# Kernel tuning notes

Measured on AMD Instinct MI355X. Metric: run time of the kernel, lower is better.

The kernel has to match this reference:

```python
import jax, jax.numpy as jnp
import numpy as np

D, N, M = 256, 8192, 8192
DISTANCE_THRESH = 0.8


def setup_inputs() -> dict:
    key = jax.random.key(0)
    k0, k1 = jax.random.split(key)
    d0 = jax.random.normal(k0, (D, N), dtype=jnp.float32)
    d1 = jax.random.normal(k1, (D, M), dtype=jnp.float32)
    # descriptors are L2-normalized along the feature dim (cosine similarity,
    # consistent with the 2*(1-sim) squared-distance formula in the module)
    d0 = d0 / jnp.linalg.norm(d0, axis=0, keepdims=True)
    d1 = d1 / jnp.linalg.norm(d1, axis=0, keepdims=True)
    return {"descriptors0": d0, "descriptors1": d1}


def reference(descriptors0, descriptors1):
    # nn_sim: [N, M] similarity matrix
    nn_sim = jnp.einsum('dn,dm->nm', descriptors0, descriptors1)
    nn_dist_01 = jnp.max(nn_sim, axis=1)          # [N]
    nn_idx_01 = jnp.argmax(nn_sim, axis=1)        # [N]
    nn_idx_10 = jnp.argmax(nn_sim, axis=0)        # [M]
    nn_dist = 2.0 * (1.0 - nn_dist_01)            # squared L2 dist for unit vecs
    ids1 = jnp.arange(nn_sim.shape[0])
    mask = ids1 == nn_idx_10[nn_idx_01]           # mutual NN check
    if DISTANCE_THRESH > 0.0:
        mask = mask & (nn_dist <= DISTANCE_THRESH ** 2)
    matches = jnp.where(mask, nn_idx_01, -1)
    scores = jnp.where(mask, (nn_dist + 1.0) / 2.0, 0.0)
    return matches, scores
```

## Files before the change

kernel.cpp:

```cpp
#include <hip/hip_runtime.h>
#include <hip/hip_bf16.h>

typedef __attribute__((ext_vector_type(8))) short short8;
typedef __attribute__((ext_vector_type(4))) float floatx4;
typedef unsigned int u32;

#define D_DIM 256
#define TCOLS 64
#define TILES 8
#define IDX_BITS 0x1FFFu
#define VAL_MASK 0xFFFFE000u


__device__ inline unsigned short f2bf_rne(float f) {
  u32 u = __float_as_uint(f);
  u32 r = (u + 0x7FFFu + ((u >> 16) & 1u)) >> 16;
  return (unsigned short)r;
}

__device__ inline u32 umax(u32 a, u32 b) { return a > b ? a : b; }

__device__ inline void async_ld16(const void* g, void* l) {
  __builtin_amdgcn_global_load_lds((const __attribute__((address_space(1))) void*)g,
                                   (__attribute__((address_space(3))) void*)l, 16, 0, 0);
}


__global__ __launch_bounds__(256) void transpose_cast(const float* __restrict__ d0,
                                                      const float* __restrict__ d1,
                                                      unsigned short* __restrict__ At,
                                                      unsigned short* __restrict__ Bt,
                                                      int C, u32* __restrict__ best, int init_n) {
  const float* src = blockIdx.z ? d1 : d0;
  unsigned short* dst = blockIdx.z ? Bt : At;
  const int tid = threadIdx.x;
  const int d = blockIdx.x * 64 + (tid & 63);
  const int chunk = blockIdx.y * 4 + (tid >> 6);
  const int f0 = chunk * 8;
  float v[8];
#pragma unroll
  for (int u = 0; u < 8; ++u) v[u] = src[(size_t)(f0 + u) * C + d];
  short8 o;
#pragma unroll
  for (int u = 0; u < 8; ++u) o[u] = (short)f2bf_rne(v[u]);
  *(short8*)(dst + (size_t)d * D_DIM + f0) = o;
  if (blockIdx.z == 0 && blockIdx.y == 0) {
    int i = blockIdx.x * 256 + tid;
    if (i < init_n) best[i] = 0u;
  }
}

__global__ __launch_bounds__(256, 1) void gemm_reduce(const unsigned short* __restrict__ At,
                                                      const unsigned short* __restrict__ Bt,
                                                      u32* __restrict__ best01,
                                                      u32* __restrict__ best10) {
  __shared__ alignas(16) unsigned short sB[2][TCOLS * D_DIM];
  __shared__ u32 ldsCol[2][TCOLS];

  const int tid  = threadIdx.x;
  const int wave = tid >> 6;
  const int lane = tid & 63;
  const int quad = lane >> 4;
  const int l15  = lane & 15;
  const int n0   = blockIdx.x * 256;
  const int mg0  = blockIdx.y * (TILES * TCOLS);
  const int rbase = n0 + wave * 64;

  if (tid < 2 * TCOLS) ldsCol[tid >> 6][tid & 63] = 0u;

  {
    const unsigned short* src = Bt + (size_t)mg0 * D_DIM;
#pragma unroll
    for (int c = 0; c < 8; ++c) {
      int slot = c * 256 + tid;
      int r = slot >> 5, cc = slot & 31;
      int ccg = (cc & 24) | ((cc ^ r) & 7);
      async_ld16(src + (size_t)r * D_DIM + ccg * 8, (unsigned short*)sB[0] + slot * 8);
    }
  }

  short8 af[4][8];
#pragma unroll
  for (int t = 0; t < 4; ++t)
#pragma unroll
    for (int kc = 0; kc < 8; ++kc)
      af[t][kc] = *(const short8*)(At + (size_t)(rbase + t * 16 + l15) * D_DIM + kc * 32 + quad * 8);

  u32 rbk[16];
#pragma unroll
  for (int s = 0; s < 16; ++s) rbk[s] = 0u;

  __syncthreads();

  for (int mt = 0; mt < TILES; ++mt) {
    const int m0 = mg0 + mt * TCOLS;
    if (mt + 1 < TILES) {
      const unsigned short* src = Bt + (size_t)(m0 + TCOLS) * D_DIM;
      unsigned short* dstb = (unsigned short*)sB[(mt + 1) & 1];
#pragma unroll
      for (int c = 0; c < 8; ++c) {
        int slot = c * 256 + tid;
        int r = slot >> 5, cc = slot & 31;
        int ccg = (cc & 24) | ((cc ^ r) & 7);
        async_ld16(src + (size_t)r * D_DIM + ccg * 8, dstb + slot * 8);
      }
    }

    floatx4 acc[4][4];
#pragma unroll
    for (int i = 0; i < 4; ++i)
#pragma unroll
      for (int j = 0; j < 4; ++j)
        acc[i][j] = (floatx4){2.0f, 2.0f, 2.0f, 2.0f};

    const unsigned short* sb = (const unsigned short*)sB[mt & 1];
#pragma unroll
    for (int kc = 0; kc < 8; ++kc) {
      short8 bfr[4];
#pragma unroll
      for (int j = 0; j < 4; ++j) {
        int c2 = j * 16 + l15;
        int ch = kc * 4 + quad;
        int chg = (ch & 24) | ((ch ^ c2) & 7);
        bfr[j] = *(const short8*)(sb + c2 * D_DIM + chg * 8);
      }
#pragma unroll
      for (int i = 0; i < 4; ++i)
#pragma unroll
        for (int j = 0; j < 4; ++j)
          acc[i][j] = __builtin_amdgcn_mfma_f32_16x16x32_bf16(af[i][kc], bfr[j], acc[i][j], 0, 0, 0);
    }

    u32 cb[4] = {0u, 0u, 0u, 0u};
    u32 colpay[4];
#pragma unroll
    for (int j = 0; j < 4; ++j) colpay[j] = (~(u32)(m0 + j * 16 + l15)) & IDX_BITS;
#pragma unroll
    for (int i = 0; i < 4; ++i)
#pragma unroll
      for (int r = 0; r < 4; ++r) {
        u32 rowpay = (~(u32)(rbase + i * 16 + quad * 4 + r)) & IDX_BITS;
        u32 rb = rbk[i * 4 + r];
#pragma unroll
        for (int j = 0; j < 4; ++j) {
          u32 u = __float_as_uint(acc[i][j][r]) & VAL_MASK;
          rb = umax(rb, u | colpay[j]);
          cb[j] = umax(cb[j], u | rowpay);
        }
        rbk[i * 4 + r] = rb;
      }
#pragma unroll
    for (int j = 0; j < 4; ++j) {
      u32 b = cb[j];
      b = umax(b, (u32)__shfl_xor((int)b, 16, 64));
      b = umax(b, (u32)__shfl_xor((int)b, 32, 64));
      if (quad == 0) atomicMax(&ldsCol[mt & 1][j * 16 + l15], b);
    }
    __syncthreads();
    if (tid < TCOLS) {
      u32 g = ldsCol[mt & 1][tid];
      ldsCol[mt & 1][tid] = 0u;
      atomicMax(&best10[m0 + tid], g);
    }
  }

#pragma unroll
  for (int i = 0; i < 4; ++i)
#pragma unroll
    for (int r = 0; r < 4; ++r) {
      u32 b = rbk[i * 4 + r];
      b = umax(b, (u32)__shfl_xor((int)b, 1, 64));
      b = umax(b, (u32)__shfl_xor((int)b, 2, 64));
      b = umax(b, (u32)__shfl_xor((int)b, 4, 64));
      b = umax(b, (u32)__shfl_xor((int)b, 8, 64));
      if (l15 == 0) atomicMax(&best01[rbase + i * 16 + quad * 4 + r], b);
    }
}

__global__ void finalize(const u32* __restrict__ best01, const u32* __restrict__ best10,
                         float* __restrict__ out, int N) {
  int n = blockIdx.x * blockDim.x + threadIdx.x;
  if (n >= N) return;
  u32 k = best01[n];
  int idx01 = (int)((~k) & IDX_BITS);
  float sim = __uint_as_float(k & VAL_MASK) - 2.0f;
  int idx10 = (int)((~best10[idx01]) & IDX_BITS);
  float dist = 2.0f - 2.0f * sim;
  bool ok = (idx10 == n) && (dist <= 0.64f);
  out[n]     = ok ? (float)idx01 : -1.0f;
  out[N + n] = ok ? 1.5f - sim : 0.0f;
}


extern "C" void kernel_launch(void* const* d_in, const int* in_sizes, int n_in,
                              void* d_out, int out_size, void* d_ws, size_t ws_size,
                              hipStream_t stream) {
  (void)n_in; (void)out_size; (void)ws_size;
  const float* d0 = (const float*)d_in[0];
  const float* d1 = (const float*)d_in[1];
  const int N = in_sizes[0] / D_DIM;
  const int M = in_sizes[1] / D_DIM;

  u32* best01 = (u32*)d_ws;
  u32* best10 = best01 + N;
  unsigned short* At = (unsigned short*)(best10 + M);
  unsigned short* Bt = At + (size_t)N * D_DIM;
  float* out = (float*)d_out;

  hipLaunchKernelGGL(transpose_cast, dim3(N / 64, 8, 2), dim3(256), 0, stream,
                     d0, d1, At, Bt, N, best01, N + M);
  hipLaunchKernelGGL(gemm_reduce, dim3(N / 256, M / (TILES * TCOLS)), dim3(256), 0, stream,
                     At, Bt, best01, best10);
  hipLaunchKernelGGL(finalize, dim3(N / 256), dim3(256), 0, stream, best01, best10, out, N);
}
```

Baseline: 122.8 us.

## Fuse descriptor0 bf16 conversion into GEMM and drop LDS column reduction

The GEMM kernel now reads descriptors0 as fp32 straight from global memory and converts it to bf16 in registers. This removes the separate transpose/cast pass and the workspace buffer for that operand; only descriptors1 is still pre-transposed. The per-block LDS stage for column maxima is also removed, so each wave issues its column-max atomics directly to global memory. The trade-offs are twice as many bytes read for A, from strided fp32 loads repeated by every column-block. Global atomic traffic on best10 is also about four times higher.

```diff
diff --git a/kernel.cpp b/kernel.cpp
--- a/kernel.cpp
+++ b/kernel.cpp
@@ -26,13 +26,9 @@
 }
 
 
-__global__ __launch_bounds__(256) void transpose_cast(const float* __restrict__ d0,
-                                                      const float* __restrict__ d1,
-                                                      unsigned short* __restrict__ At,
-                                                      unsigned short* __restrict__ Bt,
-                                                      int C, u32* __restrict__ best, int init_n) {
-  const float* src = blockIdx.z ? d1 : d0;
-  unsigned short* dst = blockIdx.z ? Bt : At;
+__global__ __launch_bounds__(256) void transpose_cast(const float* __restrict__ src,
+                                                      unsigned short* __restrict__ dst, int C,
+                                                      u32* __restrict__ best, int init_n) {
   const int tid = threadIdx.x;
   const int d = blockIdx.x * 64 + (tid & 63);
   const int chunk = blockIdx.y * 4 + (tid >> 6);
@@ -44,18 +40,18 @@
 #pragma unroll
   for (int u = 0; u < 8; ++u) o[u] = (short)f2bf_rne(v[u]);
   *(short8*)(dst + (size_t)d * D_DIM + f0) = o;
-  if (blockIdx.z == 0 && blockIdx.y == 0) {
+  if (blockIdx.y == 0) {
     int i = blockIdx.x * 256 + tid;
     if (i < init_n) best[i] = 0u;
   }
 }
 
-__global__ __launch_bounds__(256, 1) void gemm_reduce(const unsigned short* __restrict__ At,
+__global__ __launch_bounds__(256, 1) void gemm_reduce(const float* __restrict__ A,
                                                       const unsigned short* __restrict__ Bt,
                                                       u32* __restrict__ best01,
-                                                      u32* __restrict__ best10) {
+                                                      u32* __restrict__ best10,
+                                                      int N) {
   __shared__ alignas(16) unsigned short sB[2][TCOLS * D_DIM];
-  __shared__ u32 ldsCol[2][TCOLS];
 
   const int tid  = threadIdx.x;
   const int wave = tid >> 6;
@@ -66,8 +62,6 @@
   const int mg0  = blockIdx.y * (TILES * TCOLS);
   const int rbase = n0 + wave * 64;
 
-  if (tid < 2 * TCOLS) ldsCol[tid >> 6][tid & 63] = 0u;
-
   {
     const unsigned short* src = Bt + (size_t)mg0 * D_DIM;
 #pragma unroll
@@ -83,8 +77,15 @@
 #pragma unroll
   for (int t = 0; t < 4; ++t)
 #pragma unroll
-    for (int kc = 0; kc < 8; ++kc)
-      af[t][kc] = *(const short8*)(At + (size_t)(rbase + t * 16 + l15) * D_DIM + kc * 32 + quad * 8);
+    for (int kc = 0; kc < 8; ++kc) {
+      const int row = rbase + t * 16 + l15;
+      const int kb = kc * 32 + quad * 8;
+      short8 o;
+#pragma unroll
+      for (int u = 0; u < 8; ++u)
+        o[u] = (short)f2bf_rne(A[(size_t)(kb + u) * N + row]);
+      af[t][kc] = o;
+    }
 
   u32 rbk[16];
 #pragma unroll
@@ -154,14 +155,9 @@
       u32 b = cb[j];
       b = umax(b, (u32)__shfl_xor((int)b, 16, 64));
       b = umax(b, (u32)__shfl_xor((int)b, 32, 64));
-      if (quad == 0) atomicMax(&ldsCol[mt & 1][j * 16 + l15], b);
+      if (quad == 0) atomicMax(&best10[m0 + j * 16 + l15], b);
     }
     __syncthreads();
-    if (tid < TCOLS) {
-      u32 g = ldsCol[mt & 1][tid];
-      ldsCol[mt & 1][tid] = 0u;
-      atomicMax(&best10[m0 + tid], g);
-    }
   }
 
 #pragma unroll
@@ -203,13 +199,12 @@
 
   u32* best01 = (u32*)d_ws;
   u32* best10 = best01 + N;
-  unsigned short* At = (unsigned short*)(best10 + M);
-  unsigned short* Bt = At + (size_t)N * D_DIM;
+  unsigned short* Bt = (unsigned short*)(best10 + M);
   float* out = (float*)d_out;
 
-  hipLaunchKernelGGL(transpose_cast, dim3(N / 64, 8, 2), dim3(256), 0, stream,
-                     d0, d1, At, Bt, N, best01, N + M);
+  hipLaunchKernelGGL(transpose_cast, dim3(M / 64, 8), dim3(256), 0, stream,
+                     d1, Bt, M, best01, N + M);
   hipLaunchKernelGGL(gemm_reduce, dim3(N / 256, M / (TILES * TCOLS)), dim3(256), 0, stream,
-                     At, Bt, best01, best10);
+                     d0, Bt, best01, best10, N);
   hipLaunchKernelGGL(finalize, dim3(N / 256), dim3(256), 0, stream, best01, best10, out, N);
 }
```

Result: no change. 124.1 us (+1.0%).
